# Kernel optimization log

Hardware: AMD Instinct MI355X
Metric: run time of the kernel (lower is better)

The kernel has to match this reference:

```python
import jax, jax.numpy as jnp
import numpy as np
from jax import lax

B, S, D, H = 4, 1024, 1024, 16
DK = D // H


def setup_inputs() -> dict:
    key = jax.random.key(0)
    ks = jax.random.split(key, 8)
    s = 0.02
    return {
        "text_embeddings": jax.random.normal(ks[0], (B, S, D), jnp.float32),
        "text_mask": jnp.ones((B, S), jnp.int32),
        "W_G": jax.random.normal(ks[1], (D, D), jnp.float32) * s,
        "b_G": jnp.zeros((D,), jnp.float32),
        "Wq": jax.random.normal(ks[2], (D, D), jnp.float32) * s,
        "bq": jnp.zeros((D,), jnp.float32),
        "Wk": jax.random.normal(ks[3], (D, D), jnp.float32) * s,
        "bk": jnp.zeros((D,), jnp.float32),
        "conv_w": jax.random.normal(ks[4], (D, H, 3), jnp.float32) * s,
        "conv_b": jnp.zeros((D,), jnp.float32),
    }


def _rope_tables(seq_len, dk):
    # interleaved sinusoidal tables, each value repeated twice along feature dim
    pos = jnp.arange(seq_len, dtype=jnp.float32)[:, None]            # [S,1]
    inv = jnp.power(10000.0, -2.0 * jnp.arange(dk // 2, dtype=jnp.float32) / dk)
    ang = pos * inv                                                   # [S,DK/2]
    cos_pos = jnp.repeat(jnp.cos(ang), 2, axis=-1)[None, None]        # [1,1,S,DK]
    sin_pos = jnp.repeat(jnp.sin(ang), 2, axis=-1)[None, None]
    return cos_pos, sin_pos


def reference(text_embeddings, text_mask, W_G, b_G, Wq, bq, Wk, bk, conv_w, conv_b):
    b, s, d = text_embeddings.shape
    g = text_embeddings @ W_G + b_G                                   # [B,S,D]
    q = (g @ Wq + bq).reshape(b, s, H, DK).transpose(0, 2, 1, 3)      # [B,H,S,DK]
    k = (g @ Wk + bk).reshape(b, s, H, DK).transpose(0, 2, 1, 3)

    cos_pos, sin_pos = _rope_tables(s, DK)
    # NOTE: query rotation uses +q_odd (module does NOT negate for q), key uses -k_odd
    qw2 = jnp.stack([q[..., 1::2], q[..., ::2]], axis=-1).reshape(q.shape)
    qw = q * cos_pos + qw2 * sin_pos
    kw2 = jnp.stack([-k[..., 1::2], k[..., ::2]], axis=-1).reshape(k.shape)
    kw = k * cos_pos + kw2 * sin_pos

    scores = jnp.einsum("bhqd,bhkd->bhqk", qw, kw) / np.float32(np.sqrt(DK))
    mask = text_mask[:, None, None, :]                                # [B,1,1,S]
    scores = jnp.where(mask == 0, jnp.float32(-1e9), scores)
    p_attn = jax.nn.softmax(scores, axis=-1)                          # [B,H,S,S]

    row0 = p_attn[:, :, 0, :]                                         # [B,H,S]
    conv = lax.conv_general_dilated(
        row0, conv_w, window_strides=(1,), padding=[(1, 1)],
        dimension_numbers=("NCH", "OIH", "NCH"))                      # [B,D,S]
    return jax.nn.relu(conv + conv_b[None, :, None])
```

## Files before the change

kernel.cpp:

```cpp
#include <hip/hip_runtime.h>
#include <math.h>

#define B_  4
#define S_  1024
#define D_  1024
#define H_  16
#define DK_ 64
#define M_  (B_ * S_)

typedef __bf16 bf16x8 __attribute__((ext_vector_type(8)));
typedef float  f32x4  __attribute__((ext_vector_type(4)));

__device__ __forceinline__ unsigned short f2bf(float f) {
  unsigned u = __builtin_bit_cast(unsigned, f);
  u = (u + 0x7FFFu + ((u >> 16) & 1u)) >> 16;
  return (unsigned short)u;
}
__device__ __forceinline__ float bf2f(unsigned short h) {
  unsigned u = ((unsigned)h) << 16;
  return __builtin_bit_cast(float, u);
}

__device__ __forceinline__ void gl_lds16(const void* g, void* lds) {
  __builtin_amdgcn_global_load_lds(
      (const __attribute__((address_space(1))) unsigned int*)(unsigned long long)g,
      (__attribute__((address_space(3))) unsigned int*)(unsigned int)(unsigned long long)lds,
      16, 0, 0);
}

__global__ __launch_bounds__(256) void prep_kernel(
    const float* __restrict__ X, const float* __restrict__ W_G,
    const float* __restrict__ Wk, unsigned short* __restrict__ Xbf,
    unsigned short* __restrict__ WGT, unsigned short* __restrict__ WkT,
    float* __restrict__ tab) {
  __shared__ float tle[32][33];
  const int blk = blockIdx.x;
  const int tid = threadIdx.x;

  if (blk < 2048) {
    const int i = (blk * 256 + tid) * 2;
    const float4 v0 = ((const float4*)X)[i];
    const float4 v1 = ((const float4*)X)[i + 1];
    ushort4 h0, h1;
    h0.x = f2bf(v0.x); h0.y = f2bf(v0.y); h0.z = f2bf(v0.z); h0.w = f2bf(v0.w);
    h1.x = f2bf(v1.x); h1.y = f2bf(v1.y); h1.z = f2bf(v1.z); h1.w = f2bf(v1.w);
    ((ushort4*)Xbf)[i] = h0;
    ((ushort4*)Xbf)[i + 1] = h1;
  } else if (blk < 4096) {
    const bool isG = blk < 3072;
    const float* W = isG ? W_G : Wk;
    unsigned short* WT = isG ? WGT : WkT;
    const int t = isG ? blk - 2048 : blk - 3072;
    const int k0 = (t & 31) * 32;
    const int n0 = (t >> 5) * 32;
    const int tx = tid & 31;
    const int ty = tid >> 5;
#pragma unroll
    for (int r = 0; r < 32; r += 8)
      tle[ty + r][tx] = W[(size_t)(k0 + ty + r) * 1024 + n0 + tx];
    __syncthreads();
#pragma unroll
    for (int r = 0; r < 32; r += 8)
      WT[(size_t)(n0 + ty + r) * 1024 + k0 + tx] = f2bf(tle[tx][ty + r]);
  } else {
    const int idx = (blk - 4096) * 256 + tid;
    const int s = idx >> 5, j = idx & 31;
    const float inv = (float)exp(-(double)j * (9.210340371976182736 / 32.0));
    float sn, c;
    sincosf((float)s * inv, &sn, &c);
    tab[(size_t)s * 64 + 2 * j] = c;
    tab[(size_t)s * 64 + 2 * j + 1] = sn;
  }
}

#define GM 64
#define GN 128

__global__ __launch_bounds__(256) void gemm_bf16(
    const unsigned short* __restrict__ A, const unsigned short* __restrict__ BT,
    const float* __restrict__ bias, unsigned short* __restrict__ C,
    const float* __restrict__ Wq, float* __restrict__ part, int nGemmBlocks) {
  __shared__ __align__(16) unsigned short As[2][GM * 32];
  __shared__ __align__(16) unsigned short Bs[2][GN * 32];
  __shared__ float gs[4][32];

  const int flat = blockIdx.x;
  const int tid  = threadIdx.x;

  if (flat >= nGemmBlocks) {
    const int qb = flat - nGemmBlocks;
    const int slab = qb >> 2;
    const int n = (qb & 3) * 256 + tid;
    if (tid < 128) {
      const int b = tid >> 5, kk = tid & 31;
      gs[b][kk] = bf2f(A[(size_t)b * S_ * D_ + slab * 32 + kk]);
    }
    __syncthreads();
    float a0 = 0.f, a1 = 0.f, a2 = 0.f, a3 = 0.f;
#pragma unroll
    for (int kk = 0; kk < 32; ++kk) {
      const float w = Wq[(size_t)(slab * 32 + kk) * D_ + n];
      a0 = fmaf(gs[0][kk], w, a0);
      a1 = fmaf(gs[1][kk], w, a1);
      a2 = fmaf(gs[2][kk], w, a2);
      a3 = fmaf(gs[3][kk], w, a3);
    }
    part[(size_t)(slab * 4 + 0) * D_ + n] = a0;
    part[(size_t)(slab * 4 + 1) * D_ + n] = a1;
    part[(size_t)(slab * 4 + 2) * D_ + n] = a2;
    part[(size_t)(slab * 4 + 3) * D_ + n] = a3;
    return;
  }

  const int bx = flat >> 6;
  const int by = flat & 63;
  const int wv   = tid >> 6;
  const int lane = tid & 63;
  const int m0 = by * GM;
  const int n0 = bx * GN;

  const int colOff = (lane & 3) * 8;
  const size_t aOff  = (size_t)(m0 + 16 * wv + (lane >> 2)) * 1024 + colOff;
  const size_t bOff0 = (size_t)(n0 + 32 * wv + (lane >> 2)) * 1024 + colOff;
  const size_t bOff1 = bOff0 + (size_t)16 * 1024;

  const int l15  = lane & 15;
  const int quad = lane >> 4;

  f32x4 acc[4][2];
#pragma unroll
  for (int i = 0; i < 4; ++i)
#pragma unroll
    for (int j = 0; j < 2; ++j) acc[i][j] = (f32x4){0.f, 0.f, 0.f, 0.f};

#pragma unroll 1
  for (int k0 = 0; k0 < 1024; k0 += 64) {
    __syncthreads();
#pragma unroll
    for (int ks = 0; ks < 2; ++ks) {
      gl_lds16(A  + aOff  + k0 + ks * 32, &As[ks][wv * 512]);
      gl_lds16(BT + bOff0 + k0 + ks * 32, &Bs[ks][wv * 1024]);
      gl_lds16(BT + bOff1 + k0 + ks * 32, &Bs[ks][wv * 1024 + 512]);
    }
    __syncthreads();

#pragma unroll
    for (int ks = 0; ks < 2; ++ks) {
      bf16x8 af[4], bfr[2];
#pragma unroll
      for (int mi = 0; mi < 4; ++mi)
        af[mi] = *(const bf16x8*)(&As[ks][(mi * 16 + l15) * 32 + quad * 8]);
#pragma unroll
      for (int ni = 0; ni < 2; ++ni)
        bfr[ni] =
            *(const bf16x8*)(&Bs[ks][(wv * 32 + ni * 16 + l15) * 32 + quad * 8]);
#pragma unroll
      for (int mi = 0; mi < 4; ++mi)
#pragma unroll
        for (int ni = 0; ni < 2; ++ni)
          acc[mi][ni] = __builtin_amdgcn_mfma_f32_16x16x32_bf16(
              af[mi], bfr[ni], acc[mi][ni], 0, 0, 0);
    }
  }

#pragma unroll
  for (int ni = 0; ni < 2; ++ni) {
    const int n = n0 + wv * 32 + ni * 16 + l15;
    const float bv = bias[n];
#pragma unroll
    for (int mi = 0; mi < 4; ++mi) {
#pragma unroll
      for (int r = 0; r < 4; ++r) {
        const int m = m0 + mi * 16 + quad * 4 + r;
        C[(size_t)m * 1024 + n] = f2bf(acc[mi][ni][r] + bv);
      }
    }
  }
}

__global__ __launch_bounds__(256) void attn_scores_kernel(
    const unsigned short* __restrict__ Kbf, const float* __restrict__ part,
    const float* __restrict__ bq, const float* __restrict__ tab,
    const int* __restrict__ mask, float* __restrict__ scores,
    float* __restrict__ mS) {
  const int bi = blockIdx.x;
  const int b = bi >> 9;
  const int h = (bi >> 5) & 15;
  const int chunk = bi & 31;
  const int tid = threadIdx.x;
  const int bh = b * H_ + h;
  const int sl = tid >> 3;
  const int j  = tid & 7;
  const int s  = chunk * 32 + sl;

  __shared__ float q0s[DK_];
  __shared__ float wredm[4];
  __shared__ float wreds[4];

  if (tid < 64) {
    const int n = h * DK_ + tid;
    float v = bq[n];
#pragma unroll
    for (int sl2 = 0; sl2 < 32; ++sl2)
      v += part[(size_t)(sl2 * 4 + b) * D_ + n];
    q0s[tid] = v;
  }
  __syncthreads();

  const ushort4* kp =
      (const ushort4*)(Kbf + ((size_t)(b * S_ + s)) * D_ + h * DK_ + j * 8);
  const ushort4 k0 = kp[0], k1 = kp[1];
  const float4* tb = (const float4*)(tab + (size_t)s * 64 + j * 8);
  const float4 t0 = tb[0], t1 = tb[1];

  float dot = 0.f;
  {
    const float ka = bf2f(k0.x), kb = bf2f(k0.y);
    dot += q0s[j * 8 + 0] * (ka * t0.x - kb * t0.y) +
           q0s[j * 8 + 1] * (kb * t0.x + ka * t0.y);
  }
  {
    const float ka = bf2f(k0.z), kb = bf2f(k0.w);
    dot += q0s[j * 8 + 2] * (ka * t0.z - kb * t0.w) +
           q0s[j * 8 + 3] * (kb * t0.z + ka * t0.w);
  }
  {
    const float ka = bf2f(k1.x), kb = bf2f(k1.y);
    dot += q0s[j * 8 + 4] * (ka * t1.x - kb * t1.y) +
           q0s[j * 8 + 5] * (kb * t1.x + ka * t1.y);
  }
  {
    const float ka = bf2f(k1.z), kb = bf2f(k1.w);
    dot += q0s[j * 8 + 6] * (ka * t1.z - kb * t1.w) +
           q0s[j * 8 + 7] * (kb * t1.z + ka * t1.w);
  }
  dot += __shfl_xor(dot, 1);
  dot += __shfl_xor(dot, 2);
  dot += __shfl_xor(dot, 4);
  dot *= 0.125f;
  if (mask[b * S_ + s] == 0) dot = -1e9f;
  if (j == 0) scores[(size_t)bh * S_ + s] = dot;

  float mx = dot;
#pragma unroll
  for (int off = 8; off < 64; off <<= 1) mx = fmaxf(mx, __shfl_xor(mx, off));
  if ((tid & 63) == 0) wredm[tid >> 6] = mx;
  __syncthreads();
  mx = fmaxf(fmaxf(wredm[0], wredm[1]), fmaxf(wredm[2], wredm[3]));

  float e = (j == 0) ? expf(dot - mx) : 0.f;
#pragma unroll
  for (int off = 1; off < 64; off <<= 1) e += __shfl_xor(e, off);
  if ((tid & 63) == 0) wreds[tid >> 6] = e;
  __syncthreads();
  if (tid == 0) {
    mS[(size_t)(bh * 32 + chunk) * 2 + 0] = mx;
    mS[(size_t)(bh * 32 + chunk) * 2 + 1] =
        wreds[0] + wreds[1] + wreds[2] + wreds[3];
  }
}

__global__ __launch_bounds__(256) void conv_norm_relu_kernel(
    const float* __restrict__ scores, const float* __restrict__ mS,
    const float* __restrict__ cw, const float* __restrict__ cb,
    float* __restrict__ out) {
  const int b  = blockIdx.y;
  const int s0 = blockIdx.x * 64;
  const int o0 = blockIdx.z * 64;
  const int tid = threadIdx.x;

  __shared__ float msh[16], ish[16];
  __shared__ __align__(16) float wsm[64 * 48];
  __shared__ float cbs[64];
  __shared__ float sm[16][66];

  if (tid < 16) {
    const int bh = b * H_ + tid;
    float m = -3e38f;
#pragma unroll
    for (int c = 0; c < 32; ++c)
      m = fmaxf(m, mS[(size_t)(bh * 32 + c) * 2]);
    float S = 0.f;
#pragma unroll
    for (int c = 0; c < 32; ++c)
      S += mS[(size_t)(bh * 32 + c) * 2 + 1] *
           expf(mS[(size_t)(bh * 32 + c) * 2] - m);
    msh[tid] = m;
    ish[tid] = 1.f / S;
  }
  for (int i = tid; i < 64 * 48; i += 256) wsm[i] = cw[(size_t)o0 * 48 + i];
  if (tid < 64) cbs[tid] = cb[o0 + tid];
  __syncthreads();

  for (int i = tid; i < 16 * 66; i += 256) {
    const int c = i / 66, ss = i % 66;
    const int gs = s0 - 1 + ss;
    sm[c][ss] = (gs >= 0 && gs < S_)
                    ? expf(scores[(size_t)(b * H_ + c) * S_ + gs] - msh[c]) *
                          ish[c]
                    : 0.f;
  }
  __syncthreads();

  const int w = tid >> 6;
  const int l = tid & 63;
  float r[16][3];
#pragma unroll
  for (int c = 0; c < 16; ++c) {
    r[c][0] = sm[c][l + 0];
    r[c][1] = sm[c][l + 1];
    r[c][2] = sm[c][l + 2];
  }

  float* outRow = out + ((size_t)b * D_ + o0) * S_ + s0 + l;
#pragma unroll 2
  for (int i = 0; i < 16; ++i) {
    const int ol = i * 4 + w;
    const float* wr = &wsm[ol * 48];
    float acc = cbs[ol];
#pragma unroll
    for (int c = 0; c < 16; ++c) {
      acc = fmaf(r[c][0], wr[c * 3 + 0], acc);
      acc = fmaf(r[c][1], wr[c * 3 + 1], acc);
      acc = fmaf(r[c][2], wr[c * 3 + 2], acc);
    }
    outRow[(size_t)ol * S_] = fmaxf(acc, 0.f);
  }
}

extern "C" void kernel_launch(void* const* d_in, const int* in_sizes, int n_in,
                              void* d_out, int out_size, void* d_ws,
                              size_t ws_size, hipStream_t stream) {
  const float* x    = (const float*)d_in[0];
  const int*   mask = (const int*)d_in[1];
  const float* W_G  = (const float*)d_in[2];
  const float* b_G  = (const float*)d_in[3];
  const float* Wq   = (const float*)d_in[4];
  const float* bq   = (const float*)d_in[5];
  const float* Wk   = (const float*)d_in[6];
  const float* bk   = (const float*)d_in[7];
  const float* cw   = (const float*)d_in[8];
  const float* cb   = (const float*)d_in[9];
  float* out = (float*)d_out;

  char* ws = (char*)d_ws;
  unsigned short* Xbf = (unsigned short*)(ws);
  unsigned short* G   = (unsigned short*)(ws + (8u << 20));
  unsigned short* Kbf = (unsigned short*)(ws + (16u << 20));
  unsigned short* WGT = (unsigned short*)(ws + (24u << 20));
  unsigned short* WkT = (unsigned short*)(ws + (26u << 20));
  float* part   = (float*)(ws + (28u << 20));
  float* ropeT  = (float*)(ws + (28u << 20) + (512u << 10));
  float* scores = (float*)(ws + (28u << 20) + (768u << 10));
  float* mS     = (float*)(ws + (28u << 20) + (1024u << 10));

  prep_kernel<<<4224, 256, 0, stream>>>(x, W_G, Wk, Xbf, WGT, WkT, ropeT);
  gemm_bf16<<<512, 256, 0, stream>>>(Xbf, WGT, b_G, G, nullptr, nullptr, 512);
  gemm_bf16<<<640, 256, 0, stream>>>(G, WkT, bk, Kbf, Wq, part, 512);
  attn_scores_kernel<<<2048, 256, 0, stream>>>(Kbf, part, bq, ropeT, mask,
                                               scores, mS);
  conv_norm_relu_kernel<<<dim3(16, B_, 16), 256, 0, stream>>>(
      scores, mS, cw, cb, out);
}
```

Baseline: 157.1 us.

## Register-tile conv kernel with 8x8 outputs per thread and vector stores

Restructures the conv+normalize+relu kernel so each block covers 128 output channels by 128 positions. Each thread now computes an 8x8 register tile from a transposed weight tile and a normalized-probability tile in shared memory. Loads and stores use float4 vectors, which raises arithmetic per shared-memory load and widens global writes. The grid drops to a quarter of its former block count, which lowers parallelism, and the 64 accumulators per thread increase register pressure.

```diff
diff --git a/kernel.cpp b/kernel.cpp
--- a/kernel.cpp
+++ b/kernel.cpp
@@ -265,14 +265,16 @@
     const float* __restrict__ cw, const float* __restrict__ cb,
     float* __restrict__ out) {
   const int b  = blockIdx.y;
-  const int s0 = blockIdx.x * 64;
-  const int o0 = blockIdx.z * 64;
+  const int s0 = blockIdx.x * 128;
+  const int o0 = blockIdx.z * 128;
   const int tid = threadIdx.x;
+  const int tx = tid & 15;
+  const int ty = tid >> 4;
 
   __shared__ float msh[16], ish[16];
-  __shared__ __align__(16) float wsm[64 * 48];
-  __shared__ float cbs[64];
-  __shared__ float sm[16][66];
+  __shared__ __align__(16) float wT[48][128];
+  __shared__ float cbs[128];
+  __shared__ __align__(16) float pm[16][132];
 
   if (tid < 16) {
     const int bh = b * H_ + tid;
@@ -288,43 +290,61 @@
     msh[tid] = m;
     ish[tid] = 1.f / S;
   }
-  for (int i = tid; i < 64 * 48; i += 256) wsm[i] = cw[(size_t)o0 * 48 + i];
-  if (tid < 64) cbs[tid] = cb[o0 + tid];
-  __syncthreads();
-
-  for (int i = tid; i < 16 * 66; i += 256) {
-    const int c = i / 66, ss = i % 66;
+  for (int i = tid; i < 128 * 48; i += 256) {
+    const int ol = i / 48, ct = i % 48;
+    wT[ct][ol] = cw[(size_t)(o0 + ol) * 48 + ct];
+  }
+  if (tid < 128) cbs[tid] = cb[o0 + tid];
+  __syncthreads();
+
+  for (int i = tid; i < 16 * 130; i += 256) {
+    const int c = i / 130, ss = i % 130;
     const int gs = s0 - 1 + ss;
-    sm[c][ss] = (gs >= 0 && gs < S_)
+    pm[c][ss] = (gs >= 0 && gs < S_)
                     ? expf(scores[(size_t)(b * H_ + c) * S_ + gs] - msh[c]) *
                           ish[c]
                     : 0.f;
   }
   __syncthreads();
 
-  const int w = tid >> 6;
-  const int l = tid & 63;
-  float r[16][3];
+  float acc[8][8];
+#pragma unroll
+  for (int i = 0; i < 8; ++i) {
+    const float cv = cbs[ty * 8 + i];
+#pragma unroll
+    for (int j = 0; j < 8; ++j) acc[i][j] = cv;
+  }
+
 #pragma unroll
   for (int c = 0; c < 16; ++c) {
-    r[c][0] = sm[c][l + 0];
-    r[c][1] = sm[c][l + 1];
-    r[c][2] = sm[c][l + 2];
-  }
-
-  float* outRow = out + ((size_t)b * D_ + o0) * S_ + s0 + l;
-#pragma unroll 2
-  for (int i = 0; i < 16; ++i) {
-    const int ol = i * 4 + w;
-    const float* wr = &wsm[ol * 48];
-    float acc = cbs[ol];
-#pragma unroll
-    for (int c = 0; c < 16; ++c) {
-      acc = fmaf(r[c][0], wr[c * 3 + 0], acc);
-      acc = fmaf(r[c][1], wr[c * 3 + 1], acc);
-      acc = fmaf(r[c][2], wr[c * 3 + 2], acc);
-    }
-    outRow[(size_t)ol * S_] = fmaxf(acc, 0.f);
+    float p[12];
+    *(float4*)(p + 0) = *(const float4*)&pm[c][tx * 8 + 0];
+    *(float4*)(p + 4) = *(const float4*)&pm[c][tx * 8 + 4];
+    *(float4*)(p + 8) = *(const float4*)&pm[c][tx * 8 + 8];
+#pragma unroll
+    for (int t = 0; t < 3; ++t) {
+      float w[8];
+      *(float4*)(w + 0) = *(const float4*)&wT[c * 3 + t][ty * 8 + 0];
+      *(float4*)(w + 4) = *(const float4*)&wT[c * 3 + t][ty * 8 + 4];
+#pragma unroll
+      for (int i = 0; i < 8; ++i)
+#pragma unroll
+        for (int j = 0; j < 8; ++j)
+          acc[i][j] = fmaf(p[j + t], w[i], acc[i][j]);
+    }
+  }
+
+#pragma unroll
+  for (int i = 0; i < 8; ++i) {
+    float* orow =
+        out + ((size_t)b * D_ + o0 + ty * 8 + i) * S_ + s0 + tx * 8;
+    float4 v0, v1;
+    v0.x = fmaxf(acc[i][0], 0.f); v0.y = fmaxf(acc[i][1], 0.f);
+    v0.z = fmaxf(acc[i][2], 0.f); v0.w = fmaxf(acc[i][3], 0.f);
+    v1.x = fmaxf(acc[i][4], 0.f); v1.y = fmaxf(acc[i][5], 0.f);
+    v1.z = fmaxf(acc[i][6], 0.f); v1.w = fmaxf(acc[i][7], 0.f);
+    *(float4*)(orow + 0) = v0;
+    *(float4*)(orow + 4) = v1;
   }
 }
 
@@ -359,6 +379,6 @@
   gemm_bf16<<<640, 256, 0, stream>>>(G, WkT, bk, Kbf, Wq, part, 512);
   attn_scores_kernel<<<2048, 256, 0, stream>>>(Kbf, part, bq, ropeT, mask,
                                                scores, mS);
-  conv_norm_relu_kernel<<<dim3(16, B_, 16), 256, 0, stream>>>(
+  conv_norm_relu_kernel<<<dim3(8, B_, 8), 256, 0, stream>>>(
       scores, mS, cw, cb, out);
 }
```

After: 153.4 us. 2.4% less time.
